# Kernel optimization log

Measured on AMD Instinct MI355X. Metric: run time of the kernel, lower is better.

The kernel has to match this reference:

```python
import jax, jax.numpy as jnp
import numpy as np

EMBED_DIM = 1024
NUM_HEADS = 16
HEAD_DIM = EMBED_DIM // NUM_HEADS
BATCH = 4
SEQ = 2048


def setup_inputs() -> dict:
    key = jax.random.key(0)
    k1, k2, k3 = jax.random.split(key, 3)
    scale = 0.02
    x = jax.random.normal(k1, (BATCH, SEQ, EMBED_DIM), dtype=jnp.float32)
    Wqkv = jax.random.normal(k2, (EMBED_DIM, 3 * EMBED_DIM), dtype=jnp.float32) * scale
    bqkv = jnp.zeros((3 * EMBED_DIM,), dtype=jnp.float32)
    Wout = jax.random.normal(k3, (EMBED_DIM, EMBED_DIM), dtype=jnp.float32) * scale
    bout = jnp.zeros((EMBED_DIM,), dtype=jnp.float32)
    # causal mask: 1 where attention is allowed (lower triangle), 0 elsewhere
    mask = jnp.tril(jnp.ones((SEQ, SEQ), dtype=jnp.int32))
    return {"x": x, "mask": mask, "Wqkv": Wqkv, "bqkv": bqkv, "Wout": Wout, "bout": bout}


def reference(x, mask, Wqkv, bqkv, Wout, bout):
    B, S, E = x.shape
    H, D = NUM_HEADS, HEAD_DIM
    qkv = x @ Wqkv + bqkv                      # [B,S,3E]
    qkv = qkv.reshape(B, S, 3, H, D)
    qkv = jnp.transpose(qkv, (2, 0, 3, 1, 4))  # [3,B,H,S,D]
    Q, K, V = qkv[0], qkv[1], qkv[2]
    scores = jnp.einsum('bhqd,bhkd->bhqk', Q, K) / jnp.sqrt(jnp.float32(D))
    scores = jnp.where(mask[None, None] == 0, jnp.float32(-jnp.inf), scores)
    attn = jax.nn.softmax(scores, axis=-1)     # dropout omitted (eval mode)
    out = jnp.einsum('bhqk,bhkd->bhqd', attn, V)
    out = jnp.transpose(out, (0, 2, 1, 3)).reshape(B, S, E)
    return out @ Wout + bout
```

## Files before the change

### kernel.cpp

```cpp
#include <hip/hip_runtime.h>

#define S_LEN 2048
#define NH    16
#define HD    64
#define EMB   1024
#define NB    4
#define MROWS (NB * S_LEN)

typedef __attribute__((ext_vector_type(8))) short  short8;
typedef __attribute__((ext_vector_type(4))) float  float4_t;
typedef __attribute__((ext_vector_type(4))) int    int4_t;
union U8 { int4_t i; short8 s; };

__device__ __forceinline__ unsigned short f2bf(float f) {
    unsigned int x = __float_as_uint(f);
    unsigned int r = (x + 0x7fffu + ((x >> 16) & 1u)) >> 16;
    return (unsigned short)r;
}

__device__ __forceinline__ unsigned int cvtpk_bf16(float lo, float hi) {
    unsigned int r;
    asm("v_cvt_pk_bf16_f32 %0, %1, %2" : "=v"(r) : "v"(lo), "v"(hi));
    return r;
}

typedef const __attribute__((address_space(1))) unsigned int* gas_ptr;
typedef __attribute__((address_space(3))) unsigned int*       las_ptr;
__device__ __forceinline__ void gld_lds16(const void* g, void* l) {
    __builtin_amdgcn_global_load_lds((gas_ptr)g, (las_ptr)l, 16, 0, 0);
}

template<bool B> struct BoolC { static constexpr bool v = B; };

#define QSCALE 0.18033688011112042f

__global__ void cvt_f32_bf16(const float* __restrict__ in,
                             unsigned short* __restrict__ out, int n2) {
    int i = blockIdx.x * blockDim.x + threadIdx.x;
    if (i < n2) {
        float2 v = ((const float2*)in)[i];
        ushort2 o; o.x = f2bf(v.x); o.y = f2bf(v.y);
        ((ushort2*)out)[i] = o;
    }
}

__global__ void transpose_f32_bf16(const float* __restrict__ in,
                                   unsigned short* __restrict__ out, int R, int C) {
    __shared__ float tile[32][33];
    int n0 = blockIdx.x * 32, r0 = blockIdx.y * 32;
    int tx = threadIdx.x, ty = threadIdx.y;
#pragma unroll
    for (int i = 0; i < 4; ++i)
        tile[ty + i * 8][tx] = in[(size_t)(r0 + ty + i * 8) * C + n0 + tx];
    __syncthreads();
#pragma unroll
    for (int i = 0; i < 4; ++i)
        out[(size_t)(n0 + ty + i * 8) * R + r0 + tx] = f2bf(tile[tx][ty + i * 8]);
}

__global__ __launch_bounds__(256, 2) void gemm_qkv(
    const unsigned short* __restrict__ X,
    const unsigned short* __restrict__ WT,
    const float* __restrict__ bias,
    unsigned short* __restrict__ Qb,
    unsigned short* __restrict__ Kb,
    unsigned short* __restrict__ VTb)
{
    __shared__ alignas(16) unsigned short smemA[3 * 4096];
    __shared__ alignas(16) unsigned short smemB[3 * 4096];
    const int K = 1024;
    const int NT = K / 32;
    int t = threadIdx.x;
    int wave = t >> 6, lane = t & 63, quad = lane >> 4, l = lane & 15;
    int bm = blockIdx.x * 128, bn = blockIdx.y * 128;
    int wm = (wave >> 1) * 64, wn = (wave & 1) * 64;
    int colrd = (quad ^ (l & 3)) * 8;

    float4_t z = {0.f, 0.f, 0.f, 0.f};
    float4_t acc[4][4];
#pragma unroll
    for (int i = 0; i < 4; ++i)
#pragma unroll
        for (int j = 0; j < 4; ++j) acc[i][j] = z;

    auto stage = [&](int kt, int slot) {
        int k0 = kt * 32;
        unsigned short* Ad = smemA + slot * 4096;
        unsigned short* Bd = smemB + slot * 4096;
#pragma unroll
        for (int it = 0; it < 2; ++it) {
            int c = t + 256 * it;
            int row = c >> 2, col = ((c & 3) ^ (row & 3)) * 8;
            gld_lds16(&X [(size_t)(bm + row) * K + k0 + col], &Ad[c * 8]);
            gld_lds16(&WT[(size_t)(bn + row) * K + k0 + col], &Bd[c * 8]);
        }
    };

    auto compute = [&](int slot) {
        const unsigned short* Ac = smemA + slot * 4096;
        const unsigned short* Bc = smemB + slot * 4096;
        short8 af[4], bfr[4];
#pragma unroll
        for (int i = 0; i < 4; ++i)
            af[i] = *(const short8*)&Ac[(wm + i * 16 + l) * 32 + colrd];
#pragma unroll
        for (int j = 0; j < 4; ++j)
            bfr[j] = *(const short8*)&Bc[(wn + j * 16 + l) * 32 + colrd];
#pragma unroll
        for (int i = 0; i < 4; ++i)
#pragma unroll
            for (int j = 0; j < 4; ++j)
                acc[i][j] = __builtin_amdgcn_mfma_f32_16x16x32_bf16(
                    af[i], bfr[j], acc[i][j], 0, 0, 0);
    };

    stage(0, 0);
    stage(1, 1);
    int cs = 0, ss = 2;
    for (int u = 0; u < NT; ++u) {
        if (u + 1 < NT) {
            asm volatile("s_waitcnt vmcnt(4)" ::: "memory");
        } else {
            asm volatile("s_waitcnt vmcnt(0)" ::: "memory");
        }
        __builtin_amdgcn_s_barrier();
        __builtin_amdgcn_sched_barrier(0);
        if (u + 2 < NT) stage(u + 2, ss);
        compute(cs);
        cs = (cs == 2) ? 0 : cs + 1;
        ss = (ss == 2) ? 0 : ss + 1;
    }

#pragma unroll
    for (int j = 0; j < 4; ++j) {
        int gc = bn + wn + j * 16 + l;
        float bv = bias[gc];
        int which = gc >> 10, rem = gc & 1023;
        int h = rem >> 6, d = rem & 63;
        if (which == 2) {
            int bb = bm >> 11;
            size_t rowbase = ((size_t)(bb * NH + h) * HD + d) * S_LEN;
#pragma unroll
            for (int i = 0; i < 4; ++i) {
                uint2 vv;
                vv.x = cvtpk_bf16(acc[i][j][0] + bv, acc[i][j][1] + bv);
                vv.y = cvtpk_bf16(acc[i][j][2] + bv, acc[i][j][3] + bv);
                int s0 = (bm + wm + i * 16 + quad * 4) & 2047;
                int k6 = s0 & 63;
                int s0p = (s0 & ~63) | (((k6 >> 2) & 3) << 4) | (((k6 >> 4) & 3) << 2);
                *(uint2*)&VTb[rowbase + s0p] = vv;
            }
        } else {
#pragma unroll
            for (int i = 0; i < 4; ++i)
#pragma unroll
                for (int r = 0; r < 4; ++r) {
                    int gr = bm + wm + i * 16 + quad * 4 + r;
                    int b = gr >> 11, s = gr & 2047;
                    float ov = acc[i][j][r] + bv;
                    size_t bh2 = (size_t)(b * NH + h);
                    if (which == 0) Qb[(bh2 * S_LEN + s) * HD + d] = f2bf(ov * QSCALE);
                    else            Kb[(bh2 * S_LEN + s) * HD + d] = f2bf(ov);
                }
        }
    }
}

__global__ __launch_bounds__(256, 2) void flash_attn(
    const unsigned short* __restrict__ Qb,
    const unsigned short* __restrict__ Kb,
    const unsigned short* __restrict__ VTb,
    unsigned short* __restrict__ AO)
{
    __shared__ alignas(16) unsigned short smem[24576];

    int t = threadIdx.x, wave = t >> 6, lane = t & 63, quad = lane >> 4, cl = lane & 15;
    int blk = blockIdx.x;
    int bh = (blk & 7) + 8 * ((blk >> 3) & 7);
    int g = blk >> 6;
    int b = bh >> 4, h = bh & 15;
    int ci = (wave & 2) ? (62 - 2 * g + (wave & 1)) : (2 * g + (wave & 1));
    int qb = 32 * ci;
    int nkt = (ci >> 1) + 1;
    int nkt_max = 32 - g;

    const unsigned short* Qbase = Qb  + (size_t)bh * S_LEN * HD;
    const unsigned short* Kbase = Kb  + (size_t)bh * S_LEN * HD;
    const unsigned short* Vbase = VTb + (size_t)bh * HD * S_LEN;

    float4_t z = {0.f, 0.f, 0.f, 0.f};
    short8 onesf;
#pragma unroll
    for (int i = 0; i < 8; ++i) onesf[i] = (short)0x3F80;

    short8 bQ[2][2];
#pragma unroll
    for (int qt = 0; qt < 2; ++qt)
#pragma unroll
        for (int hh = 0; hh < 2; ++hh)
            bQ[qt][hh] = *(const short8*)&Qbase[(size_t)(qb + qt * 16 + cl) * HD + hh * 32 + quad * 8];

    float4_t acc[2][4], accs[2];
#pragma unroll
    for (int qt = 0; qt < 2; ++qt) {
        accs[qt] = z;
#pragma unroll
        for (int nb = 0; nb < 4; ++nb) acc[qt][nb] = z;
    }

    int koff0[4], koff1[4];
#pragma unroll
    for (int t4 = 0; t4 < 4; ++t4) {
        int row = t4 * 16 + cl, sw = row & 7;
        koff0[t4] = (row << 7) | ((quad ^ sw) << 4);
        koff1[t4] = (row << 7) | (((quad + 4) ^ sw) << 4);
    }
    int voffB[2][4];
#pragma unroll
    for (int p = 0; p < 2; ++p)
#pragma unroll
        for (int nb = 0; nb < 4; ++nb) {
            int row = nb * 16 + cl;
            voffB[p][nb] = 8192 + ((row << 7) | (((quad * 2 + p) ^ (row & 7)) << 4));
        }

    auto stage = [&](int kt, int slot) {
        int key0 = kt << 6;
        unsigned short* Kd = smem + slot * 8192;
        unsigned short* Vd = Kd + 4096;
#pragma unroll
        for (int i = 0; i < 2; ++i) {
            int s = t + 256 * i;
            int row = s >> 3, c16 = (s & 7) ^ (row & 7);
            gld_lds16(&Kbase[(size_t)(key0 + row) * HD + c16 * 8], &Kd[s * 8]);
            gld_lds16(&Vbase[(size_t)row * S_LEN + key0 + c16 * 8], &Vd[s * 8]);
        }
    };

    auto compute = [&](auto DIAGC, int slot, int key0) {
        constexpr bool DIAG = decltype(DIAGC)::v;
        const char* Kc = (const char*)(smem + slot * 8192);
        short8 aK0[4], aK1[4];
#pragma unroll
        for (int t4 = 0; t4 < 4; ++t4) {
            aK0[t4] = *(const short8*)(Kc + koff0[t4]);
            aK1[t4] = *(const short8*)(Kc + koff1[t4]);
        }
        U8 bv[2][4];
#pragma unroll
        for (int p = 0; p < 2; ++p)
#pragma unroll
            for (int nb = 0; nb < 4; ++nb)
                bv[p][nb].i = *(const int4_t*)(Kc + voffB[p][nb]);

#pragma unroll
        for (int qt = 0; qt < 2; ++qt) {
            unsigned int pk[4][2];
#pragma unroll
            for (int t4 = 0; t4 < 4; ++t4) {
                float4_t st = __builtin_amdgcn_mfma_f32_16x16x32_bf16(
                    aK1[t4], bQ[qt][1],
                    __builtin_amdgcn_mfma_f32_16x16x32_bf16(aK0[t4], bQ[qt][0], z, 0, 0, 0),
                    0, 0, 0);
                float e[4];
#pragma unroll
                for (int r = 0; r < 4; ++r) {
                    e[r] = __builtin_amdgcn_exp2f(st[r]);
                    if (DIAG) {
                        int key = key0 + t4 * 16 + quad * 4 + r;
                        e[r] = (key <= qb + qt * 16 + cl) ? e[r] : 0.f;
                    }
                }
                pk[t4][0] = cvtpk_bf16(e[0], e[1]);
                pk[t4][1] = cvtpk_bf16(e[2], e[3]);
            }
#pragma unroll
            for (int p = 0; p < 2; ++p) {
                U8 a; a.i = (int4_t){(int)pk[2 * p][0], (int)pk[2 * p][1],
                                     (int)pk[2 * p + 1][0], (int)pk[2 * p + 1][1]};
                accs[qt] = __builtin_amdgcn_mfma_f32_16x16x32_bf16(
                    a.s, onesf, accs[qt], 0, 0, 0);
#pragma unroll
                for (int nb = 0; nb < 4; ++nb)
                    acc[qt][nb] = __builtin_amdgcn_mfma_f32_16x16x32_bf16(
                        a.s, bv[p][nb].s, acc[qt][nb], 0, 0, 0);
            }
        }
    };

    stage(0, 0);
    if (nkt_max > 1) stage(1, 1);
    int cb = 0, sb = 2;
    for (int u = 0; u < nkt_max; ++u) {
        if (u + 1 < nkt_max) {
            asm volatile("s_waitcnt vmcnt(4)" ::: "memory");
        } else {
            asm volatile("s_waitcnt vmcnt(0)" ::: "memory");
        }
        __builtin_amdgcn_s_barrier();
        __builtin_amdgcn_sched_barrier(0);
        if (u + 2 < nkt_max) stage(u + 2, sb);
        if (u < nkt) {
            if (u == nkt - 1) compute(BoolC<true>{},  cb, u << 6);
            else              compute(BoolC<false>{}, cb, u << 6);
        }
        cb = (cb == 2) ? 0 : cb + 1;
        sb = (sb == 2) ? 0 : sb + 1;
    }

    __syncthreads();
    unsigned short* stgw = smem + wave * 1088;

#pragma unroll
    for (int qt = 0; qt < 2; ++qt) {
        float fr[4];
#pragma unroll
        for (int r = 0; r < 4; ++r) fr[r] = 1.f / accs[qt][r];
#pragma unroll
        for (int nb = 0; nb < 4; ++nb)
#pragma unroll
            for (int r = 0; r < 4; ++r) {
                unsigned int uu = __float_as_uint(acc[qt][nb][r] * fr[r]) + 0x8000u;
                stgw[(quad * 4 + r) * 68 + nb * 16 + cl] = (unsigned short)(uu >> 16);
            }
#pragma unroll
        for (int pass = 0; pass < 4; ++pass) {
            int idx = pass * 64 + lane;
            int row = idx >> 4, part = idx & 15;
            ushort4 v = *(const ushort4*)&stgw[row * 68 + part * 4];
            *(ushort4*)&AO[((size_t)b * S_LEN + qb + qt * 16 + row) * EMB + h * HD + part * 4] = v;
        }
    }
}

__global__ __launch_bounds__(256, 2) void gemm_out(
    const unsigned short* __restrict__ A,
    const unsigned short* __restrict__ WT,
    const float* __restrict__ bias,
    float* __restrict__ out)
{
    __shared__ alignas(16) unsigned short smemA[3 * 4096];
    __shared__ alignas(16) unsigned short smemB[3 * 4096];
    const int K = 1024;
    const int NT = K / 32;
    int t = threadIdx.x;
    int wave = t >> 6, lane = t & 63, quad = lane >> 4, l = lane & 15;
    int bm = blockIdx.x * 128, bn = blockIdx.y * 128;
    int wm = (wave >> 1) * 64, wn = (wave & 1) * 64;
    int colrd = (quad ^ (l & 3)) * 8;

    float4_t z = {0.f, 0.f, 0.f, 0.f};
    float4_t acc[4][4];
#pragma unroll
    for (int i = 0; i < 4; ++i)
#pragma unroll
        for (int j = 0; j < 4; ++j) acc[i][j] = z;

    auto stage = [&](int kt, int slot) {
        int k0 = kt * 32;
        unsigned short* Ad = smemA + slot * 4096;
        unsigned short* Bd = smemB + slot * 4096;
#pragma unroll
        for (int it = 0; it < 2; ++it) {
            int c = t + 256 * it;
            int row = c >> 2, col = ((c & 3) ^ (row & 3)) * 8;
            gld_lds16(&A [(size_t)(bm + row) * K + k0 + col], &Ad[c * 8]);
            gld_lds16(&WT[(size_t)(bn + row) * K + k0 + col], &Bd[c * 8]);
        }
    };

    auto compute = [&](int slot) {
        const unsigned short* Ac = smemA + slot * 4096;
        const unsigned short* Bc = smemB + slot * 4096;
        short8 af[4], bfr[4];
#pragma unroll
        for (int i = 0; i < 4; ++i)
            af[i] = *(const short8*)&Ac[(wm + i * 16 + l) * 32 + colrd];
#pragma unroll
        for (int j = 0; j < 4; ++j)
            bfr[j] = *(const short8*)&Bc[(wn + j * 16 + l) * 32 + colrd];
#pragma unroll
        for (int i = 0; i < 4; ++i)
#pragma unroll
            for (int j = 0; j < 4; ++j)
                acc[i][j] = __builtin_amdgcn_mfma_f32_16x16x32_bf16(
                    af[i], bfr[j], acc[i][j], 0, 0, 0);
    };

    stage(0, 0);
    stage(1, 1);
    int cs = 0, ss = 2;
    for (int u = 0; u < NT; ++u) {
        if (u + 1 < NT) {
            asm volatile("s_waitcnt vmcnt(4)" ::: "memory");
        } else {
            asm volatile("s_waitcnt vmcnt(0)" ::: "memory");
        }
        __builtin_amdgcn_s_barrier();
        __builtin_amdgcn_sched_barrier(0);
        if (u + 2 < NT) stage(u + 2, ss);
        compute(cs);
        cs = (cs == 2) ? 0 : cs + 1;
        ss = (ss == 2) ? 0 : ss + 1;
    }

#pragma unroll
    for (int j = 0; j < 4; ++j) {
        int gc = bn + wn + j * 16 + l;
        float bv = bias[gc];
#pragma unroll
        for (int i = 0; i < 4; ++i) {
#pragma unroll
            for (int r = 0; r < 4; ++r) {
                int gr = bm + wm + i * 16 + quad * 4 + r;
                out[(size_t)gr * EMB + gc] = acc[i][j][r] + bv;
            }
        }
    }
}

extern "C" void kernel_launch(void* const* d_in, const int* in_sizes, int n_in,
                              void* d_out, int out_size, void* d_ws, size_t ws_size,
                              hipStream_t stream) {
    const float* x    = (const float*)d_in[0];
    const float* Wqkv = (const float*)d_in[2];
    const float* bqkv = (const float*)d_in[3];
    const float* Wout = (const float*)d_in[4];
    const float* bout = (const float*)d_in[5];
    float* out = (float*)d_out;

    char* ws = (char*)d_ws;
    const size_t SZ = (size_t)NB * NH * S_LEN * HD * 2;
    unsigned short* Qb    = (unsigned short*)(ws);
    unsigned short* Kb    = (unsigned short*)(ws + SZ);
    unsigned short* VTb   = (unsigned short*)(ws + 2 * SZ);
    unsigned short* Xb    = (unsigned short*)(ws + 3 * SZ);
    unsigned short* AO    = (unsigned short*)(ws + 3 * SZ);
    unsigned short* WqkvT = (unsigned short*)(ws + 4 * SZ);
    unsigned short* WoutT = (unsigned short*)(ws + 4 * SZ + (size_t)3 * EMB * EMB * 2);

    int n2 = MROWS * EMB / 2;
    cvt_f32_bf16<<<dim3((n2 + 255) / 256), 256, 0, stream>>>(x, Xb, n2);
    dim3 tb(32, 8);
    transpose_f32_bf16<<<dim3(3 * EMB / 32, EMB / 32), tb, 0, stream>>>(Wqkv, WqkvT, EMB, 3 * EMB);
    transpose_f32_bf16<<<dim3(EMB / 32, EMB / 32), tb, 0, stream>>>(Wout, WoutT, EMB, EMB);
    gemm_qkv<<<dim3(MROWS / 128, 3 * EMB / 128), 256, 0, stream>>>(Xb, WqkvT, bqkv, Qb, Kb, VTb);
    flash_attn<<<dim3(1024), 256, 0, stream>>>(Qb, Kb, VTb, AO);
    gemm_out<<<dim3(MROWS / 128, EMB / 128), 256, 0, stream>>>(AO, WoutT, bout, out);
}
```

Before: 254.6 us.

## Stage QKV GEMM epilogue through LDS for coalesced stores and fuse prep kernels

The QKV GEMM epilogue now writes bias-added bf16 results into shared memory, then emits 16-byte coalesced stores to Q, K and the permuted V-transpose layout, replacing scattered 2-byte stores. The three conversion/transpose prep kernels are merged into one launch. The LDS swizzle pattern in both GEMMs is changed to a different XOR scheme to reduce bank conflicts. The extra barriers and LDS round trip add some epilogue cost.

New measurement: 240.9 us. -5.4%, faster.

```diff
diff --git a/kernel.cpp b/kernel.cpp
--- a/kernel.cpp
+++ b/kernel.cpp
@@ -34,21 +34,31 @@
 
 #define QSCALE 0.18033688011112042f
 
-__global__ void cvt_f32_bf16(const float* __restrict__ in,
-                             unsigned short* __restrict__ out, int n2) {
-    int i = blockIdx.x * blockDim.x + threadIdx.x;
-    if (i < n2) {
-        float2 v = ((const float2*)in)[i];
+__global__ __launch_bounds__(256) void prep(
+    const float* __restrict__ x,    unsigned short* __restrict__ Xb,
+    const float* __restrict__ Wqkv, unsigned short* __restrict__ WqkvT,
+    const float* __restrict__ Wout, unsigned short* __restrict__ WoutT)
+{
+    __shared__ float tile[32][33];
+    int bid = blockIdx.x, t = threadIdx.x;
+    if (bid < 16384) {
+        int i = bid * 256 + t;
+        float2 v = ((const float2*)x)[i];
         ushort2 o; o.x = f2bf(v.x); o.y = f2bf(v.y);
-        ((ushort2*)out)[i] = o;
-    }
-}
-
-__global__ void transpose_f32_bf16(const float* __restrict__ in,
-                                   unsigned short* __restrict__ out, int R, int C) {
-    __shared__ float tile[32][33];
-    int n0 = blockIdx.x * 32, r0 = blockIdx.y * 32;
-    int tx = threadIdx.x, ty = threadIdx.y;
+        ((ushort2*)Xb)[i] = o;
+        return;
+    }
+    const float* in; unsigned short* out; int R, C, n0, r0;
+    if (bid < 19456) {
+        int b2 = bid - 16384;
+        in = Wqkv; out = WqkvT; R = EMB; C = 3 * EMB;
+        n0 = (b2 % 96) * 32; r0 = (b2 / 96) * 32;
+    } else {
+        int b2 = bid - 19456;
+        in = Wout; out = WoutT; R = EMB; C = EMB;
+        n0 = (b2 & 31) * 32; r0 = (b2 >> 5) * 32;
+    }
+    int tx = t & 31, ty = t >> 5;
 #pragma unroll
     for (int i = 0; i < 4; ++i)
         tile[ty + i * 8][tx] = in[(size_t)(r0 + ty + i * 8) * C + n0 + tx];
@@ -66,15 +76,14 @@
     unsigned short* __restrict__ Kb,
     unsigned short* __restrict__ VTb)
 {
-    __shared__ alignas(16) unsigned short smemA[3 * 4096];
-    __shared__ alignas(16) unsigned short smemB[3 * 4096];
+    __shared__ alignas(16) unsigned short smem[24576];
     const int K = 1024;
     const int NT = K / 32;
     int t = threadIdx.x;
     int wave = t >> 6, lane = t & 63, quad = lane >> 4, l = lane & 15;
     int bm = blockIdx.x * 128, bn = blockIdx.y * 128;
     int wm = (wave >> 1) * 64, wn = (wave & 1) * 64;
-    int colrd = (quad ^ (l & 3)) * 8;
+    int colrd = (quad ^ ((l >> 1) & 3)) * 8;
 
     float4_t z = {0.f, 0.f, 0.f, 0.f};
     float4_t acc[4][4];
@@ -85,20 +94,21 @@
 
     auto stage = [&](int kt, int slot) {
         int k0 = kt * 32;
-        unsigned short* Ad = smemA + slot * 4096;
-        unsigned short* Bd = smemB + slot * 4096;
+        unsigned short* Ad = smem + slot * 4096;
+        unsigned short* Bd = smem + 12288 + slot * 4096;
 #pragma unroll
         for (int it = 0; it < 2; ++it) {
             int c = t + 256 * it;
-            int row = c >> 2, col = ((c & 3) ^ (row & 3)) * 8;
+            int row = c >> 2;
+            int col = ((c & 3) ^ ((c >> 3) & 3)) * 8;
             gld_lds16(&X [(size_t)(bm + row) * K + k0 + col], &Ad[c * 8]);
             gld_lds16(&WT[(size_t)(bn + row) * K + k0 + col], &Bd[c * 8]);
         }
     };
 
     auto compute = [&](int slot) {
-        const unsigned short* Ac = smemA + slot * 4096;
-        const unsigned short* Bc = smemB + slot * 4096;
+        const unsigned short* Ac = smem + slot * 4096;
+        const unsigned short* Bc = smem + 12288 + slot * 4096;
         short8 af[4], bfr[4];
 #pragma unroll
         for (int i = 0; i < 4; ++i)
@@ -131,37 +141,61 @@
         ss = (ss == 2) ? 0 : ss + 1;
     }
 
-#pragma unroll
-    for (int j = 0; j < 4; ++j) {
-        int gc = bn + wn + j * 16 + l;
-        float bv = bias[gc];
-        int which = gc >> 10, rem = gc & 1023;
-        int h = rem >> 6, d = rem & 63;
-        if (which == 2) {
-            int bb = bm >> 11;
-            size_t rowbase = ((size_t)(bb * NH + h) * HD + d) * S_LEN;
+    __syncthreads();
+    int which = bn >> 10;
+    int bnr = bn & 1023;
+    int b = bm >> 11;
+    if (which == 2) {
+#pragma unroll
+        for (int j = 0; j < 4; ++j) {
+            float bv = bias[bn + wn + j * 16 + l];
+            int c = wn + j * 16 + l;
 #pragma unroll
             for (int i = 0; i < 4; ++i) {
                 uint2 vv;
                 vv.x = cvtpk_bf16(acc[i][j][0] + bv, acc[i][j][1] + bv);
                 vv.y = cvtpk_bf16(acc[i][j][2] + bv, acc[i][j][3] + bv);
-                int s0 = (bm + wm + i * 16 + quad * 4) & 2047;
-                int k6 = s0 & 63;
-                int s0p = (s0 & ~63) | (((k6 >> 2) & 3) << 4) | (((k6 >> 4) & 3) << 2);
-                *(uint2*)&VTb[rowbase + s0p] = vv;
+                *(uint2*)&smem[c * 132 + wm + quad * 16 + i * 4] = vv;
             }
-        } else {
+        }
+        __syncthreads();
+        int sbase = bm & 2047;
+#pragma unroll
+        for (int pass = 0; pass < 8; ++pass) {
+            int c = pass * 16 + (t >> 4);
+            int sp = (t & 15) * 8;
+            int rem = bnr + c, h = rem >> 6, d = rem & 63;
+            uint2 lo = *(const uint2*)&smem[c * 132 + sp];
+            uint2 hi = *(const uint2*)&smem[c * 132 + sp + 4];
+            int4_t v = {(int)lo.x, (int)lo.y, (int)hi.x, (int)hi.y};
+            *(int4_t*)&VTb[((size_t)(b * NH + h) * HD + d) * S_LEN + sbase + sp] = v;
+        }
+    } else {
+#pragma unroll
+        for (int j = 0; j < 4; ++j) {
+            float bv = bias[bn + wn + j * 16 + l];
+            int c = wn + j * 16 + l;
 #pragma unroll
             for (int i = 0; i < 4; ++i)
 #pragma unroll
                 for (int r = 0; r < 4; ++r) {
-                    int gr = bm + wm + i * 16 + quad * 4 + r;
-                    int b = gr >> 11, s = gr & 2047;
                     float ov = acc[i][j][r] + bv;
-                    size_t bh2 = (size_t)(b * NH + h);
-                    if (which == 0) Qb[(bh2 * S_LEN + s) * HD + d] = f2bf(ov * QSCALE);
-                    else            Kb[(bh2 * S_LEN + s) * HD + d] = f2bf(ov);
+                    if (which == 0) ov *= QSCALE;
+                    smem[(wm + i * 16 + quad * 4 + r) * 132 + c] = f2bf(ov);
                 }
+        }
+        __syncthreads();
+        unsigned short* dst = which ? Kb : Qb;
+        int s0g = bm & 2047;
+#pragma unroll
+        for (int pass = 0; pass < 8; ++pass) {
+            int s = pass * 16 + (t >> 4);
+            int cp = (t & 15) * 8;
+            int rem = bnr + cp, h = rem >> 6, d = rem & 63;
+            uint2 lo = *(const uint2*)&smem[s * 132 + cp];
+            uint2 hi = *(const uint2*)&smem[s * 132 + cp + 4];
+            int4_t v = {(int)lo.x, (int)lo.y, (int)hi.x, (int)hi.y};
+            *(int4_t*)&dst[((size_t)(b * NH + h) * S_LEN + s0g + s) * HD + d] = v;
         }
     }
 }
@@ -347,7 +381,7 @@
     int wave = t >> 6, lane = t & 63, quad = lane >> 4, l = lane & 15;
     int bm = blockIdx.x * 128, bn = blockIdx.y * 128;
     int wm = (wave >> 1) * 64, wn = (wave & 1) * 64;
-    int colrd = (quad ^ (l & 3)) * 8;
+    int colrd = (quad ^ ((l >> 1) & 3)) * 8;
 
     float4_t z = {0.f, 0.f, 0.f, 0.f};
     float4_t acc[4][4];
@@ -363,7 +397,8 @@
 #pragma unroll
         for (int it = 0; it < 2; ++it) {
             int c = t + 256 * it;
-            int row = c >> 2, col = ((c & 3) ^ (row & 3)) * 8;
+            int row = c >> 2;
+            int col = ((c & 3) ^ ((c >> 3) & 3)) * 8;
             gld_lds16(&A [(size_t)(bm + row) * K + k0 + col], &Ad[c * 8]);
             gld_lds16(&WT[(size_t)(bn + row) * K + k0 + col], &Bd[c * 8]);
         }
@@ -439,11 +474,7 @@
     unsigned short* WqkvT = (unsigned short*)(ws + 4 * SZ);
     unsigned short* WoutT = (unsigned short*)(ws + 4 * SZ + (size_t)3 * EMB * EMB * 2);
 
-    int n2 = MROWS * EMB / 2;
-    cvt_f32_bf16<<<dim3((n2 + 255) / 256), 256, 0, stream>>>(x, Xb, n2);
-    dim3 tb(32, 8);
-    transpose_f32_bf16<<<dim3(3 * EMB / 32, EMB / 32), tb, 0, stream>>>(Wqkv, WqkvT, EMB, 3 * EMB);
-    transpose_f32_bf16<<<dim3(EMB / 32, EMB / 32), tb, 0, stream>>>(Wout, WoutT, EMB, EMB);
+    prep<<<dim3(20480), 256, 0, stream>>>(x, Xb, Wqkv, WqkvT, Wout, WoutT);
     gemm_qkv<<<dim3(MROWS / 128, 3 * EMB / 128), 256, 0, stream>>>(Xb, WqkvT, bqkv, Qb, Kb, VTb);
     flash_attn<<<dim3(1024), 256, 0, stream>>>(Qb, Kb, VTb, AO);
     gemm_out<<<dim3(MROWS / 128, EMB / 128), 256, 0, stream>>>(AO, WoutT, bout, out);
```
